# Kernel optimization log

Hardware: AMD Instinct MI355X
Metric: run time of the kernel (lower is better)

Reference implementation:

```python
import jax, jax.numpy as jnp
import numpy as np

D = 1024; HEADS = 16; DH = D // HEADS; DEPTH = 8; FACT = 2
EPS = 1e-6


def _rmsnorm(x):
    return x * jax.lax.rsqrt(jnp.mean(x * x, axis=-1, keepdims=True) + EPS)


def _rope(x, pos):
    # x: [N, H, T, d]; pos: [T]. Standard rotate-half RoPE on dim d.
    d = x.shape[-1]
    half = d // 2
    inv_freq = 1.0 / (10000.0 ** (jnp.arange(half, dtype=x.dtype) / half))
    ang = pos[:, None] * inv_freq  # [T, half]
    cos = jnp.concatenate([jnp.cos(ang), jnp.cos(ang)], axis=-1)  # [T, d]
    sin = jnp.concatenate([jnp.sin(ang), jnp.sin(ang)], axis=-1)
    rot = jnp.concatenate([-x[..., half:], x[..., :half]], axis=-1)
    return x * cos + rot * sin


def _apply_rope_2d(q, k, pos_h, pos_w):
    # Split head_dim in half: first half rotated by row position, second by column.
    dh = q.shape[-1] // 2
    q = jnp.concatenate([_rope(q[..., :dh], pos_h), _rope(q[..., dh:], pos_w)], axis=-1)
    k = jnp.concatenate([_rope(k[..., :dh], pos_h), _rope(k[..., dh:], pos_w)], axis=-1)
    return q, k


def setup_inputs() -> dict:
    key = jax.random.key(0)
    ks = jax.random.split(key, 8)
    s = 0.02
    f32 = jnp.float32
    return {
        "x": jax.random.normal(ks[0], (4, 16, 64, 64), f32),
        "merge_w": (jax.random.normal(ks[1], (D, 16 * FACT * FACT), f32) * s),
        "qkv_w": (jax.random.normal(ks[2], (DEPTH, 3 * D, D), f32) * s),
        "qkv_b": jnp.zeros((DEPTH, 3 * D), f32),
        "proj_w": (jax.random.normal(ks[3], (DEPTH, D, D), f32) * s),
        "proj_b": jnp.zeros((DEPTH, D), f32),
        "fc1_w": (jax.random.normal(ks[4], (DEPTH, 4 * D, D), f32) * s),
        "fc1_b": jnp.zeros((DEPTH, 4 * D), f32),
        "fc2_w": (jax.random.normal(ks[5], (DEPTH, D, 4 * D), f32) * s),
        "fc2_b": jnp.zeros((DEPTH, D), f32),
    }


def reference(x, merge_w, qkv_w, qkv_b, proj_w, proj_b, fc1_w, fc1_b, fc2_w, fc2_b):
    N, C, H, W = x.shape
    Hf, Wf = H // FACT, W // FACT
    L = Hf * Wf
    # SpatialMerger: unfold(k=f,s=f) channel order is (c, kh, kw)
    patches = x.reshape(N, C, Hf, FACT, Wf, FACT)
    patches = patches.transpose(0, 2, 4, 1, 3, 5).reshape(N, L, C * FACT * FACT)
    tok = patches @ merge_w.T  # [N, L, D], bias=False

    pos_h = jnp.repeat(jnp.arange(Hf, dtype=tok.dtype), Wf)  # [L]
    pos_w = jnp.tile(jnp.arange(Wf, dtype=tok.dtype), Hf)
    scale = 1.0 / np.sqrt(DH)

    for i in range(DEPTH):
        h = _rmsnorm(tok)
        qkv = h @ qkv_w[i].T + qkv_b[i]  # [N, L, 3D]
        q, k, v = jnp.split(qkv, 3, axis=-1)
        q = q.reshape(N, L, HEADS, DH).transpose(0, 2, 1, 3)  # [N, Hh, T, Dh]
        k = k.reshape(N, L, HEADS, DH).transpose(0, 2, 1, 3)
        v = v.reshape(N, L, HEADS, DH).transpose(0, 2, 1, 3)
        q, k = _apply_rope_2d(q, k, pos_h, pos_w)
        attn = jnp.einsum('nhtd,nhsd->nhts', q, k) * scale
        p = jax.nn.softmax(attn, axis=-1)
        o = jnp.einsum('nhts,nhsd->nhtd', p, v)
        o = o.transpose(0, 2, 1, 3).reshape(N, L, D)
        tok = tok + (o @ proj_w[i].T + proj_b[i])

        h = _rmsnorm(tok)
        hidden = jax.nn.gelu(h @ fc1_w[i].T + fc1_b[i], approximate=True)
        tok = tok + (hidden @ fc2_w[i].T + fc2_b[i])

    z_seq = _rmsnorm(tok)          # [N, L, D]
    z = z_seq.transpose(0, 2, 1)   # [N, D, L]
    return z
```

## Files before the change

### kernel.cpp

```cpp
#include <hip/hip_runtime.h>
#include <hip/hip_bf16.h>
#include <cmath>

typedef __bf16 bf16_t;
typedef __bf16 bf16x4 __attribute__((ext_vector_type(4)));
typedef __bf16 bf16x8 __attribute__((ext_vector_type(8)));
typedef float f32x4 __attribute__((ext_vector_type(4)));

typedef const __attribute__((address_space(1))) void gv_t;
typedef __attribute__((address_space(3))) void sv_t;

#define GLDS16(g, l) __builtin_amdgcn_global_load_lds((gv_t*)(g), (sv_t*)(l), 16, 0, 0)

template <int EPI>
__global__ __launch_bounds__(256, 2) void gemm128(
    const bf16_t* __restrict__ A, const bf16_t* __restrict__ B,
    const float* __restrict__ bias, float* __restrict__ Cf,
    bf16_t* __restrict__ Cb, int N, int K)
{
    __shared__ __align__(16) bf16_t As[128 * 32];
    __shared__ __align__(16) bf16_t Bs[128 * 32];
    const int tid = threadIdx.x;
    const int bm = blockIdx.x, bn = blockIdx.y;
    const int wave = tid >> 6, lane = tid & 63;
    const int wr = (wave >> 1) << 6, wc = (wave & 1) << 6;
    const int lr = lane & 15, kq = (lane >> 4) << 3;

    f32x4 acc[4][4] = {};

    const bf16_t* gA = A + (size_t)(bm * 128 + (tid >> 2)) * K + (tid & 3) * 8;
    const bf16_t* gB = B + (size_t)(bn * 128 + (tid >> 2)) * K + (tid & 3) * 8;
    const bf16_t* gA2 = gA + (size_t)64 * K;
    const bf16_t* gB2 = gB + (size_t)64 * K;
    bf16_t* lA = As + tid * 8;
    bf16_t* lB = Bs + tid * 8;

    for (int k0 = 0; k0 < K; k0 += 32) {
        __syncthreads();
        GLDS16(gA + k0, lA);
        GLDS16(gA2 + k0, lA + 2048);
        GLDS16(gB + k0, lB);
        GLDS16(gB2 + k0, lB + 2048);
        __syncthreads();
        bf16x8 af[4], bfr[4];
#pragma unroll
        for (int i = 0; i < 4; i++)
            af[i] = *(const bf16x8*)(As + (wr + i * 16 + lr) * 32 + kq);
#pragma unroll
        for (int j = 0; j < 4; j++)
            bfr[j] = *(const bf16x8*)(Bs + (wc + j * 16 + lr) * 32 + kq);
#pragma unroll
        for (int i = 0; i < 4; i++)
#pragma unroll
            for (int j = 0; j < 4; j++)
                acc[i][j] = __builtin_amdgcn_mfma_f32_16x16x32_bf16(af[i], bfr[j], acc[i][j], 0, 0, 0);
    }

    const int row0 = bm * 128 + wr + ((lane >> 4) << 2);
    const int col0 = bn * 128 + wc + lr;
#pragma unroll
    for (int j = 0; j < 4; j++) {
        const int col = col0 + j * 16;
        float bv = 0.f;
        if constexpr (EPI != 0) bv = bias[col];
#pragma unroll
        for (int i = 0; i < 4; i++) {
#pragma unroll
            for (int r = 0; r < 4; r++) {
                const int row = row0 + i * 16 + r;
                float v = acc[i][j][r] + bv;
                if constexpr (EPI == 0 || EPI == 1) {
                    Cf[(size_t)row * N + col] = v;
                } else if constexpr (EPI == 2) {
                    Cf[(size_t)row * 1024 + col] += v;
                } else if constexpr (EPI == 3) {
                    float g = 0.5f * v * (1.f + tanhf(0.7978845608f * (v + 0.044715f * v * v * v)));
                    Cb[(size_t)row * N + col] = (bf16_t)g;
                } else {
                    Cb[(size_t)row * N + col] = (bf16_t)v;
                }
            }
        }
    }
}

__global__ __launch_bounds__(256) void convw_k(
    const float* __restrict__ q, const float* __restrict__ p,
    const float* __restrict__ f1, const float* __restrict__ f2,
    bf16_t* __restrict__ oq, bf16_t* __restrict__ op,
    bf16_t* __restrict__ of1, bf16_t* __restrict__ of2)
{
    int idx = blockIdx.x * 256 + threadIdx.x;
    const float* src; bf16_t* dst; int off;
    if (idx < 786432)       { src = q;  dst = oq;  off = idx; }
    else if (idx < 1048576) { src = p;  dst = op;  off = idx - 786432; }
    else if (idx < 2097152) { src = f1; dst = of1; off = idx - 1048576; }
    else                    { src = f2; dst = of2; off = idx - 2097152; }
    float4 v = ((const float4*)src)[off];
    bf16x4 o; o[0] = (bf16_t)v.x; o[1] = (bf16_t)v.y; o[2] = (bf16_t)v.z; o[3] = (bf16_t)v.w;
    *(bf16x4*)(dst + (size_t)off * 4) = o;
}

__global__ __launch_bounds__(256) void cvt_k(const float* __restrict__ in, bf16_t* __restrict__ out)
{
    int idx = blockIdx.x * 256 + threadIdx.x;
    float4 v = ((const float4*)in)[idx];
    bf16x4 o; o[0] = (bf16_t)v.x; o[1] = (bf16_t)v.y; o[2] = (bf16_t)v.z; o[3] = (bf16_t)v.w;
    *(bf16x4*)(out + (size_t)idx * 4) = o;
}

__global__ __launch_bounds__(256) void patches_k(const float* __restrict__ x, bf16_t* __restrict__ out)
{
    int idx = blockIdx.x * 256 + threadIdx.x;
    int cc = idx & 63, l = (idx >> 6) & 1023, n = idx >> 16;
    int c = cc >> 2, kh = (cc >> 1) & 1, kw = cc & 1;
    int hf = l >> 5, wf = l & 31;
    out[idx] = (bf16_t)x[(((n * 16 + c) * 64) + hf * 2 + kh) * 64 + wf * 2 + kw];
}

__global__ __launch_bounds__(256) void rmsnorm_k(const float* __restrict__ tok, bf16_t* __restrict__ out)
{
    int row = blockIdx.x, tid = threadIdx.x;
    float4 xv = ((const float4*)(tok + (size_t)row * 1024))[tid];
    float s = xv.x * xv.x + xv.y * xv.y + xv.z * xv.z + xv.w * xv.w;
#pragma unroll
    for (int off = 32; off > 0; off >>= 1) s += __shfl_down(s, off, 64);
    __shared__ float ws4[4];
    if ((tid & 63) == 0) ws4[tid >> 6] = s;
    __syncthreads();
    float sc = rsqrtf((ws4[0] + ws4[1] + ws4[2] + ws4[3]) * (1.f / 1024.f) + 1e-6f);
    bf16_t* o = out + (size_t)row * 1024 + tid * 4;
    bf16x4 ov;
    ov[0] = (bf16_t)(xv.x * sc); ov[1] = (bf16_t)(xv.y * sc);
    ov[2] = (bf16_t)(xv.z * sc); ov[3] = (bf16_t)(xv.w * sc);
    *(bf16x4*)o = ov;
}

__global__ __launch_bounds__(256) void rope_k(bf16_t* __restrict__ qkv)
{
    int idx = blockIdx.x * 256 + threadIdx.x;
    int j = idx & 31, h = (idx >> 5) & 15, t = (idx >> 9) & 1023, n = idx >> 19;
    int b = j >> 4, jj = j & 15;
    float pos = (float)(b ? (t & 31) : (t >> 5));
    float ang = pos * exp2f(-13.287712379549449f * (float)jj * (1.f / 16.f));
    float sn, cs;
    sincosf(ang, &sn, &cs);
    bf16_t* qp = qkv + (size_t)(n * 1024 + t) * 3072 + h * 64 + b * 32 + jj;
    float q0 = (float)qp[0], q1 = (float)qp[16];
    qp[0]  = (bf16_t)(q0 * cs - q1 * sn);
    qp[16] = (bf16_t)(q1 * cs + q0 * sn);
    bf16_t* kp = qp + 1024;
    float k0 = (float)kp[0], k1 = (float)kp[16];
    kp[0]  = (bf16_t)(k0 * cs - k1 * sn);
    kp[16] = (bf16_t)(k1 * cs + k0 * sn);
}

__global__ __launch_bounds__(256) void vtrans_k(const bf16_t* __restrict__ qkv, bf16_t* __restrict__ vt)
{
    __shared__ bf16_t tile[64][72];
    const int tid = threadIdx.x, b = blockIdx.x;
    const int tt = b & 15, h = (b >> 4) & 15, n = b >> 8;
#pragma unroll
    for (int rr = 0; rr < 2; rr++) {
        int idx = rr * 256 + tid;
        int tr = idx >> 3, dc = (idx & 7) * 8;
        bf16x8 v = *(const bf16x8*)(qkv + (size_t)(n * 1024 + tt * 64 + tr) * 3072 + 2048 + h * 64 + dc);
        *(bf16x8*)&tile[tr][dc] = v;
    }
    __syncthreads();
#pragma unroll
    for (int rr = 0; rr < 2; rr++) {
        int idx = rr * 256 + tid;
        int d = idx >> 3, tc = (idx & 7) * 8;
        bf16x8 ov;
#pragma unroll
        for (int e = 0; e < 8; e++) ov[e] = tile[tc + e][d];
        *(bf16x8*)(vt + (size_t)((n * 16 + h) * 64 + d) * 1024 + tt * 64 + tc) = ov;
    }
}

__global__ __launch_bounds__(256, 2) void attn_mfma(
    const bf16_t* __restrict__ qkv, const bf16_t* __restrict__ vt, bf16_t* __restrict__ obuf)
{
    __shared__ __align__(16) bf16_t Ks[64 * 64];
    __shared__ __align__(16) bf16_t Vs[64 * 64];
    __shared__ __align__(16) bf16_t Ps[4][32 * 64];

    const int tid = threadIdx.x, wave = tid >> 6, lane = tid & 63;
    const int lr = lane & 15, g = lane >> 4;
    const int blk = blockIdx.x;
    const int qb = blk & 7, h = (blk >> 3) & 15, n = blk >> 7;
    const int t0 = qb * 128 + wave * 32;

    bf16x8 bq[2][2];
#pragma unroll
    for (int j = 0; j < 2; j++)
#pragma unroll
        for (int kk = 0; kk < 2; kk++) {
            bf16x8 v = *(const bf16x8*)(qkv + (size_t)(n * 1024 + t0 + j * 16 + lr) * 3072 + h * 64 + kk * 32 + g * 8);
#pragma unroll
            for (int e = 0; e < 8; e++) v[e] = (bf16_t)((float)v[e] * 0.125f);
            bq[j][kk] = v;
        }

    f32x4 o[2][4] = {};
    float m[2] = {-1e30f, -1e30f}, l[2] = {0.f, 0.f};

    const int sr = tid >> 3, pcb = tid & 7;
    const int scb = (pcb ^ (sr & 7)) * 8;
    const bf16_t* ksrc = qkv + (size_t)(n * 1024 + sr) * 3072 + 1024 + h * 64 + scb;
    const bf16_t* vsrc = vt + (size_t)((n * 16 + h) * 64 + sr) * 1024 + scb;
    bf16_t* kdst = Ks + tid * 8;
    bf16_t* vdst = Vs + tid * 8;

    for (int s0 = 0; s0 < 1024; s0 += 64) {
        __syncthreads();
        GLDS16(ksrc + (size_t)s0 * 3072, kdst);
        GLDS16(ksrc + (size_t)(s0 + 32) * 3072, kdst + 2048);
        GLDS16(vsrc + s0, vdst);
        GLDS16(vsrc + s0 + (size_t)32 * 1024, vdst + 2048);
        __syncthreads();

        f32x4 st[4][2] = {};
#pragma unroll
        for (int kk = 0; kk < 2; kk++) {
            bf16x8 ak[4];
#pragma unroll
            for (int i = 0; i < 4; i++)
                ak[i] = *(const bf16x8*)((const char*)Ks + (i * 16 + lr) * 128 + (((kk * 4 + g) ^ (lr & 7)) * 16));
#pragma unroll
            for (int i = 0; i < 4; i++)
#pragma unroll
                for (int j = 0; j < 2; j++)
                    st[i][j] = __builtin_amdgcn_mfma_f32_16x16x32_bf16(ak[i], bq[j][kk], st[i][j], 0, 0, 0);
        }

        float al2[2];
#pragma unroll
        for (int j = 0; j < 2; j++) {
            float rm = st[0][j][0];
#pragma unroll
            for (int i = 0; i < 4; i++)
#pragma unroll
                for (int r = 0; r < 4; r++) rm = fmaxf(rm, st[i][j][r]);
            rm = fmaxf(rm, __shfl_xor(rm, 16, 64));
            rm = fmaxf(rm, __shfl_xor(rm, 32, 64));
            float mn = fmaxf(m[j], rm);
            float al = __expf(m[j] - mn);
            m[j] = mn; al2[j] = al;
            float ps = 0.f;
#pragma unroll
            for (int i = 0; i < 4; i++) {
                bf16x4 pk;
#pragma unroll
                for (int r = 0; r < 4; r++) {
                    float p = __expf(st[i][j][r] - mn);
                    bf16_t pb = (bf16_t)p;
                    pk[r] = pb;
                    ps += (float)pb;
                }
                *(bf16x4*)((char*)&Ps[wave][0] + (j * 16 + lr) * 128 +
                           (((i * 2 + (g >> 1)) ^ (lr & 7)) * 16) + (g & 1) * 8) = pk;
            }
            ps += __shfl_xor(ps, 16, 64);
            ps += __shfl_xor(ps, 32, 64);
            l[j] = l[j] * al + ps;
        }

#pragma unroll
        for (int ti = 0; ti < 2; ti++)
#pragma unroll
            for (int r = 0; r < 4; r++) {
                float av = __shfl(al2[ti], g * 4 + r, 64);
#pragma unroll
                for (int dj = 0; dj < 4; dj++) o[ti][dj][r] *= av;
            }

#pragma unroll
        for (int kk = 0; kk < 2; kk++) {
            bf16x8 ap[2], bv[4];
#pragma unroll
            for (int ti = 0; ti < 2; ti++)
                ap[ti] = *(const bf16x8*)((const char*)&Ps[wave][0] + (ti * 16 + lr) * 128 +
                                          (((kk * 4 + g) ^ (lr & 7)) * 16));
#pragma unroll
            for (int dj = 0; dj < 4; dj++)
                bv[dj] = *(const bf16x8*)((const char*)Vs + (dj * 16 + lr) * 128 +
                                          (((kk * 4 + g) ^ (lr & 7)) * 16));
#pragma unroll
            for (int ti = 0; ti < 2; ti++)
#pragma unroll
                for (int dj = 0; dj < 4; dj++)
                    o[ti][dj] = __builtin_amdgcn_mfma_f32_16x16x32_bf16(ap[ti], bv[dj], o[ti][dj], 0, 0, 0);
        }
    }

#pragma unroll
    for (int ti = 0; ti < 2; ti++)
#pragma unroll
        for (int r = 0; r < 4; r++) {
            float lv = __shfl(l[ti], g * 4 + r, 64);
            float inv = 1.f / lv;
            const int trow = n * 1024 + qb * 128 + wave * 32 + ti * 16 + g * 4 + r;
#pragma unroll
            for (int dj = 0; dj < 4; dj++)
                obuf[(size_t)trow * 1024 + h * 64 + dj * 16 + lr] = (bf16_t)(o[ti][dj][r] * inv);
        }
}

__global__ __launch_bounds__(256) void rmsscale_k(const float* __restrict__ tok, float* __restrict__ scale)
{
    int row = blockIdx.x, tid = threadIdx.x;
    float4 xv = ((const float4*)(tok + (size_t)row * 1024))[tid];
    float s = xv.x * xv.x + xv.y * xv.y + xv.z * xv.z + xv.w * xv.w;
#pragma unroll
    for (int off = 32; off > 0; off >>= 1) s += __shfl_down(s, off, 64);
    __shared__ float ws4[4];
    if ((tid & 63) == 0) ws4[tid >> 6] = s;
    __syncthreads();
    if (tid == 0)
        scale[row] = rsqrtf((ws4[0] + ws4[1] + ws4[2] + ws4[3]) * (1.f / 1024.f) + 1e-6f);
}

__global__ __launch_bounds__(256) void transpose_out_k(const float* __restrict__ tok,
                                                       const float* __restrict__ scale,
                                                       float* __restrict__ out)
{
    __shared__ float tile[64][65];
    const int tid = threadIdx.x;
    const int tt = blockIdx.x * 64, dd = blockIdx.y * 64, n = blockIdx.z;
#pragma unroll
    for (int rb = 0; rb < 4; rb++) {
        int tl = rb * 16 + (tid >> 4);
        int cl = (tid & 15) * 4;
        float4 v = *(const float4*)(tok + (size_t)(n * 1024 + tt + tl) * 1024 + dd + cl);
        float sc = scale[n * 1024 + tt + tl];
        tile[cl + 0][tl] = v.x * sc;
        tile[cl + 1][tl] = v.y * sc;
        tile[cl + 2][tl] = v.z * sc;
        tile[cl + 3][tl] = v.w * sc;
    }
    __syncthreads();
#pragma unroll
    for (int rb = 0; rb < 4; rb++) {
        int dl = rb * 16 + (tid >> 4);
        int tl = (tid & 15) * 4;
        float4 v = make_float4(tile[dl][tl + 0], tile[dl][tl + 1], tile[dl][tl + 2], tile[dl][tl + 3]);
        *(float4*)(out + (size_t)n * 1024 * 1024 + (size_t)(dd + dl) * 1024 + tt + tl) = v;
    }
}

extern "C" void kernel_launch(void* const* d_in, const int* in_sizes, int n_in,
                              void* d_out, int out_size, void* d_ws, size_t ws_size,
                              hipStream_t stream)
{
    const float* x       = (const float*)d_in[0];
    const float* merge_w = (const float*)d_in[1];
    const float* qkv_w   = (const float*)d_in[2];
    const float* qkv_b   = (const float*)d_in[3];
    const float* proj_w  = (const float*)d_in[4];
    const float* proj_b  = (const float*)d_in[5];
    const float* fc1_w   = (const float*)d_in[6];
    const float* fc1_b   = (const float*)d_in[7];
    const float* fc2_w   = (const float*)d_in[8];
    const float* fc2_b   = (const float*)d_in[9];
    float* out = (float*)d_out;

    char* ws = (char*)d_ws;
    float*  tok   = (float*)ws;
    bf16_t* Ab    = (bf16_t*)(ws + (16u << 20));
    bf16_t* ob    = (bf16_t*)(ws + (24u << 20));
    bf16_t* qkvb  = (bf16_t*)(ws + (32u << 20));
    bf16_t* vtb   = (bf16_t*)(ws + (56u << 20));
    bf16_t* hid   = (bf16_t*)(ws + (32u << 20));
    bf16_t* wqkv  = (bf16_t*)(ws + (64u << 20));
    bf16_t* wproj = wqkv + (size_t)3072 * 1024;
    bf16_t* wfc1  = wproj + (size_t)1024 * 1024;
    bf16_t* wfc2  = wfc1 + (size_t)4096 * 1024;
    bf16_t* wmrg  = (bf16_t*)(ws + (90u << 20));
    float*  scl   = (float*)(ws + (91u << 20));

    cvt_k<<<64, 256, 0, stream>>>(merge_w, wmrg);
    patches_k<<<1024, 256, 0, stream>>>(x, Ab);
    gemm128<0><<<dim3(32, 8), 256, 0, stream>>>(Ab, wmrg, nullptr, tok, nullptr, 1024, 64);

    for (int i = 0; i < 8; i++) {
        convw_k<<<12288, 256, 0, stream>>>(
            qkv_w + (size_t)i * 3072 * 1024, proj_w + (size_t)i * 1024 * 1024,
            fc1_w + (size_t)i * 4096 * 1024, fc2_w + (size_t)i * 1024 * 4096,
            wqkv, wproj, wfc1, wfc2);

        rmsnorm_k<<<4096, 256, 0, stream>>>(tok, Ab);
        gemm128<4><<<dim3(32, 24), 256, 0, stream>>>(Ab, wqkv, qkv_b + (size_t)i * 3072,
                                                     nullptr, qkvb, 3072, 1024);
        rope_k<<<8192, 256, 0, stream>>>(qkvb);
        vtrans_k<<<1024, 256, 0, stream>>>(qkvb, vtb);
        attn_mfma<<<512, 256, 0, stream>>>(qkvb, vtb, ob);
        gemm128<2><<<dim3(32, 8), 256, 0, stream>>>(ob, wproj, proj_b + (size_t)i * 1024,
                                                    tok, nullptr, 1024, 1024);
        rmsnorm_k<<<4096, 256, 0, stream>>>(tok, Ab);
        gemm128<3><<<dim3(32, 32), 256, 0, stream>>>(Ab, wfc1, fc1_b + (size_t)i * 4096,
                                                     nullptr, hid, 4096, 1024);
        gemm128<2><<<dim3(32, 8), 256, 0, stream>>>(hid, wfc2, fc2_b + (size_t)i * 1024,
                                                    tok, nullptr, 1024, 4096);
    }
    rmsscale_k<<<4096, 256, 0, stream>>>(tok, scl);
    transpose_out_k<<<dim3(16, 16, 4), 256, 0, stream>>>(tok, scl, out);
}
```

Before: 2.591 ms.

## Triple-buffer GEMM loads, split-K residual GEMMs with atomics, fuse RoPE into QKV

The GEMM now keeps three LDS buffers and issues async global-to-LDS loads two tiles ahead, waiting with vmcnt so memory latency overlaps MFMA work. The proj and fc2 GEMMs, whose 256-block grids underfill the device, are split along K into two slices that add into the residual with float atomics. RoPE moves into the QKV GEMM epilogue, which removes a separate read-modify-write pass over q and k. The costs are more LDS per block, which may lower occupancy, nondeterministic float summation order from the atomics, and sincos work inside the GEMM epilogue.

```diff
diff --git a/kernel.cpp b/kernel.cpp
--- a/kernel.cpp
+++ b/kernel.cpp
@@ -16,63 +16,110 @@
 __global__ __launch_bounds__(256, 2) void gemm128(
     const bf16_t* __restrict__ A, const bf16_t* __restrict__ B,
     const float* __restrict__ bias, float* __restrict__ Cf,
-    bf16_t* __restrict__ Cb, int N, int K)
-{
-    __shared__ __align__(16) bf16_t As[128 * 32];
-    __shared__ __align__(16) bf16_t Bs[128 * 32];
+    bf16_t* __restrict__ Cb, int N, int K, int KS)
+{
+    __shared__ __align__(16) bf16_t As[3][128 * 32];
+    __shared__ __align__(16) bf16_t Bs[3][128 * 32];
     const int tid = threadIdx.x;
-    const int bm = blockIdx.x, bn = blockIdx.y;
+    const int bm = blockIdx.x, bn = blockIdx.y, bz = blockIdx.z;
     const int wave = tid >> 6, lane = tid & 63;
     const int wr = (wave >> 1) << 6, wc = (wave & 1) << 6;
     const int lr = lane & 15, kq = (lane >> 4) << 3;
 
     f32x4 acc[4][4] = {};
 
-    const bf16_t* gA = A + (size_t)(bm * 128 + (tid >> 2)) * K + (tid & 3) * 8;
-    const bf16_t* gB = B + (size_t)(bn * 128 + (tid >> 2)) * K + (tid & 3) * 8;
+    const int kbeg = bz * KS;
+    const bf16_t* gA = A + (size_t)(bm * 128 + (tid >> 2)) * K + (tid & 3) * 8 + kbeg;
+    const bf16_t* gB = B + (size_t)(bn * 128 + (tid >> 2)) * K + (tid & 3) * 8 + kbeg;
     const bf16_t* gA2 = gA + (size_t)64 * K;
     const bf16_t* gB2 = gB + (size_t)64 * K;
-    bf16_t* lA = As + tid * 8;
-    bf16_t* lB = Bs + tid * 8;
-
-    for (int k0 = 0; k0 < K; k0 += 32) {
-        __syncthreads();
-        GLDS16(gA + k0, lA);
-        GLDS16(gA2 + k0, lA + 2048);
-        GLDS16(gB + k0, lB);
-        GLDS16(gB2 + k0, lB + 2048);
-        __syncthreads();
+    const int dst = tid * 8;
+    const int nt = KS >> 5;
+
+#define STAGE(buf, t) do { const int _k = (t) << 5;          \
+        GLDS16(gA  + _k, As[buf] + dst);                     \
+        GLDS16(gA2 + _k, As[buf] + dst + 2048);              \
+        GLDS16(gB  + _k, Bs[buf] + dst);                     \
+        GLDS16(gB2 + _k, Bs[buf] + dst + 2048); } while (0)
+
+    STAGE(0, 0);
+    if (nt > 1) STAGE(1, 1);
+    int cur = 0, pre = 2;
+    for (int t = 0; t < nt; ++t) {
+        if (t + 1 < nt) asm volatile("s_waitcnt vmcnt(4)" ::: "memory");
+        else            asm volatile("s_waitcnt vmcnt(0)" ::: "memory");
+        __builtin_amdgcn_s_barrier();
+        if (t + 2 < nt) STAGE(pre, t + 2);
+
+        const bf16_t* Ac = As[cur];
+        const bf16_t* Bc = Bs[cur];
         bf16x8 af[4], bfr[4];
 #pragma unroll
         for (int i = 0; i < 4; i++)
-            af[i] = *(const bf16x8*)(As + (wr + i * 16 + lr) * 32 + kq);
+            af[i] = *(const bf16x8*)(Ac + (wr + i * 16 + lr) * 32 + kq);
 #pragma unroll
         for (int j = 0; j < 4; j++)
-            bfr[j] = *(const bf16x8*)(Bs + (wc + j * 16 + lr) * 32 + kq);
+            bfr[j] = *(const bf16x8*)(Bc + (wc + j * 16 + lr) * 32 + kq);
 #pragma unroll
         for (int i = 0; i < 4; i++)
 #pragma unroll
             for (int j = 0; j < 4; j++)
                 acc[i][j] = __builtin_amdgcn_mfma_f32_16x16x32_bf16(af[i], bfr[j], acc[i][j], 0, 0, 0);
-    }
+
+        cur = (cur == 2) ? 0 : cur + 1;
+        pre = (pre == 2) ? 0 : pre + 1;
+    }
+#undef STAGE
 
     const int row0 = bm * 128 + wr + ((lane >> 4) << 2);
     const int col0 = bn * 128 + wc + lr;
+
+    if constexpr (EPI == 6) {
+        float bv[4];
+#pragma unroll
+        for (int j = 0; j < 4; j++) bv[j] = bias[col0 + j * 16];
+        const bool doRope = (col0 < 2048);
+        const float invf = exp2f(-0.83048202372184056f * (float)lr);
+#pragma unroll
+        for (int i = 0; i < 4; i++) {
+#pragma unroll
+            for (int r = 0; r < 4; r++) {
+                const int row = row0 + i * 16 + r;
+                float v0 = acc[i][0][r] + bv[0], v1 = acc[i][1][r] + bv[1];
+                float v2 = acc[i][2][r] + bv[2], v3 = acc[i][3][r] + bv[3];
+                if (doRope) {
+                    const int tt = row & 1023;
+                    float s0, c0, s1, c1;
+                    sincosf((float)(tt >> 5) * invf, &s0, &c0);
+                    sincosf((float)(tt & 31) * invf, &s1, &c1);
+                    float o0 = v0 * c0 - v1 * s0, o1 = v1 * c0 + v0 * s0;
+                    float o2 = v2 * c1 - v3 * s1, o3 = v3 * c1 + v2 * s1;
+                    v0 = o0; v1 = o1; v2 = o2; v3 = o3;
+                }
+                bf16_t* cp = Cb + (size_t)row * N + col0;
+                cp[0] = (bf16_t)v0; cp[16] = (bf16_t)v1;
+                cp[32] = (bf16_t)v2; cp[48] = (bf16_t)v3;
+            }
+        }
+        return;
+    }
+
 #pragma unroll
     for (int j = 0; j < 4; j++) {
         const int col = col0 + j * 16;
         float bv = 0.f;
-        if constexpr (EPI != 0) bv = bias[col];
+        if constexpr (EPI == 5) { if (bz == 0) bv = bias[col]; }
+        else if constexpr (EPI != 0) bv = bias[col];
 #pragma unroll
         for (int i = 0; i < 4; i++) {
 #pragma unroll
             for (int r = 0; r < 4; r++) {
                 const int row = row0 + i * 16 + r;
                 float v = acc[i][j][r] + bv;
-                if constexpr (EPI == 0 || EPI == 1) {
+                if constexpr (EPI == 0) {
                     Cf[(size_t)row * N + col] = v;
-                } else if constexpr (EPI == 2) {
-                    Cf[(size_t)row * 1024 + col] += v;
+                } else if constexpr (EPI == 5) {
+                    atomicAdd(&Cf[(size_t)row * 1024 + col], v);
                 } else if constexpr (EPI == 3) {
                     float g = 0.5f * v * (1.f + tanhf(0.7978845608f * (v + 0.044715f * v * v * v)));
                     Cb[(size_t)row * N + col] = (bf16_t)g;
@@ -134,25 +181,6 @@
     ov[0] = (bf16_t)(xv.x * sc); ov[1] = (bf16_t)(xv.y * sc);
     ov[2] = (bf16_t)(xv.z * sc); ov[3] = (bf16_t)(xv.w * sc);
     *(bf16x4*)o = ov;
-}
-
-__global__ __launch_bounds__(256) void rope_k(bf16_t* __restrict__ qkv)
-{
-    int idx = blockIdx.x * 256 + threadIdx.x;
-    int j = idx & 31, h = (idx >> 5) & 15, t = (idx >> 9) & 1023, n = idx >> 19;
-    int b = j >> 4, jj = j & 15;
-    float pos = (float)(b ? (t & 31) : (t >> 5));
-    float ang = pos * exp2f(-13.287712379549449f * (float)jj * (1.f / 16.f));
-    float sn, cs;
-    sincosf(ang, &sn, &cs);
-    bf16_t* qp = qkv + (size_t)(n * 1024 + t) * 3072 + h * 64 + b * 32 + jj;
-    float q0 = (float)qp[0], q1 = (float)qp[16];
-    qp[0]  = (bf16_t)(q0 * cs - q1 * sn);
-    qp[16] = (bf16_t)(q1 * cs + q0 * sn);
-    bf16_t* kp = qp + 1024;
-    float k0 = (float)kp[0], k1 = (float)kp[16];
-    kp[0]  = (bf16_t)(k0 * cs - k1 * sn);
-    kp[16] = (bf16_t)(k1 * cs + k0 * sn);
 }
 
 __global__ __launch_bounds__(256) void vtrans_k(const bf16_t* __restrict__ qkv, bf16_t* __restrict__ vt)
@@ -382,7 +410,7 @@
 
     cvt_k<<<64, 256, 0, stream>>>(merge_w, wmrg);
     patches_k<<<1024, 256, 0, stream>>>(x, Ab);
-    gemm128<0><<<dim3(32, 8), 256, 0, stream>>>(Ab, wmrg, nullptr, tok, nullptr, 1024, 64);
+    gemm128<0><<<dim3(32, 8, 1), 256, 0, stream>>>(Ab, wmrg, nullptr, tok, nullptr, 1024, 64, 64);
 
     for (int i = 0; i < 8; i++) {
         convw_k<<<12288, 256, 0, stream>>>(
@@ -391,18 +419,17 @@
             wqkv, wproj, wfc1, wfc2);
 
         rmsnorm_k<<<4096, 256, 0, stream>>>(tok, Ab);
-        gemm128<4><<<dim3(32, 24), 256, 0, stream>>>(Ab, wqkv, qkv_b + (size_t)i * 3072,
-                                                     nullptr, qkvb, 3072, 1024);
-        rope_k<<<8192, 256, 0, stream>>>(qkvb);
+        gemm128<6><<<dim3(32, 24, 1), 256, 0, stream>>>(Ab, wqkv, qkv_b + (size_t)i * 3072,
+                                                        nullptr, qkvb, 3072, 1024, 1024);
         vtrans_k<<<1024, 256, 0, stream>>>(qkvb, vtb);
         attn_mfma<<<512, 256, 0, stream>>>(qkvb, vtb, ob);
-        gemm128<2><<<dim3(32, 8), 256, 0, stream>>>(ob, wproj, proj_b + (size_t)i * 1024,
-                                                    tok, nullptr, 1024, 1024);
+        gemm128<5><<<dim3(32, 8, 2), 256, 0, stream>>>(ob, wproj, proj_b + (size_t)i * 1024,
+                                                       tok, nullptr, 1024, 1024, 512);
         rmsnorm_k<<<4096, 256, 0, stream>>>(tok, Ab);
-        gemm128<3><<<dim3(32, 32), 256, 0, stream>>>(Ab, wfc1, fc1_b + (size_t)i * 4096,
-                                                     nullptr, hid, 4096, 1024);
-        gemm128<2><<<dim3(32, 8), 256, 0, stream>>>(hid, wfc2, fc2_b + (size_t)i * 1024,
-                                                    tok, nullptr, 1024, 4096);
+        gemm128<3><<<dim3(32, 32, 1), 256, 0, stream>>>(Ab, wfc1, fc1_b + (size_t)i * 4096,
+                                                        nullptr, hid, 4096, 1024, 1024);
+        gemm128<5><<<dim3(32, 8, 2), 256, 0, stream>>>(hid, wfc2, fc2_b + (size_t)i * 1024,
+                                                       tok, nullptr, 1024, 4096, 2048);
     }
     rmsscale_k<<<4096, 256, 0, stream>>>(tok, scl);
     transpose_out_k<<<dim3(16, 16, 4), 256, 0, stream>>>(tok, scl, out);
```

New measurement: 2.514 ms. 3.0% less time.
